# Performance work log

Measured on AMD Instinct MI355X. Metric: run time of the kernel, lower is better.

The kernel has to match this reference:

```python
import jax, jax.numpy as jnp
import numpy as np

N_NODES = 100000

def _gcn_norm(edge_index, num_nodes):
    # PyG GCNConv: add self-loops, symmetric normalization deg^-1/2 A_hat deg^-1/2
    loop = jnp.arange(num_nodes, dtype=edge_index.dtype)
    src = jnp.concatenate([edge_index[0], loop])  # [E+N]
    dst = jnp.concatenate([edge_index[1], loop])  # [E+N]
    deg = jax.ops.segment_sum(jnp.ones(dst.shape[0], jnp.float32), dst, num_segments=num_nodes)
    dis = jnp.where(deg > 0, jax.lax.rsqrt(deg), 0.0)
    norm = dis[src] * dis[dst]  # [E+N]
    return src, dst, norm

def _gcn_layer(x, W, b, src, dst, norm, num_nodes):
    xw = x @ W                                   # [N, H] dense GEMM first (out_dim <= in_dim)
    msg = xw[src] * norm[:, None]                # gather + scale per edge
    out = jax.ops.segment_sum(msg, dst, num_segments=num_nodes)  # scatter-add
    return out + b

def setup_inputs() -> dict:
    key = jax.random.key(0)
    ks = jax.random.split(key, 6)
    E = 1600000
    return {
        "x": jax.random.normal(ks[0], (N_NODES, 512), jnp.float32),
        "edge_index": jax.random.randint(ks[1], (2, E), 0, N_NODES, dtype=jnp.int64),
        "W1": jax.random.normal(ks[2], (512, 256), jnp.float32) * 0.04,
        "b1": jnp.zeros((256,), jnp.float32),
        "W2": jax.random.normal(ks[3], (256, 256), jnp.float32) * 0.06,
        "b2": jnp.zeros((256,), jnp.float32),
        "fc_w": jax.random.normal(ks[4], (256, 128), jnp.float32) * 0.06,
        "fc_b": jnp.zeros((128,), jnp.float32),
    }

def reference(x, edge_index, W1, b1, W2, b2, fc_w, fc_b):
    src, dst, norm = _gcn_norm(edge_index, N_NODES)
    h = jax.nn.relu(_gcn_layer(x, W1, b1, src, dst, norm, N_NODES))
    h = jax.nn.relu(_gcn_layer(h, W2, b2, src, dst, norm, N_NODES))
    return h @ fc_w + fc_b
```

## Files before the change

kernel.cpp:

```cpp
#include <hip/hip_runtime.h>


#define N_NODES 100000
constexpr int D_IN  = 512;
constexpr int D_H   = 256;
constexpr int D_OUT = 128;
constexpr int M_PAD = 100096;

typedef _Float16 f16x8 __attribute__((ext_vector_type(8)));
typedef _Float16 f16x4 __attribute__((ext_vector_type(4)));
typedef float f32x4 __attribute__((ext_vector_type(4)));

#define GLD16(SRC, DST) __builtin_amdgcn_global_load_lds(                      \
    (const __attribute__((address_space(1))) void*)(SRC),                      \
    (__attribute__((address_space(3))) void*)(DST), 16, 0, 0)

__global__ __launch_bounds__(256) void cvt_x_k(const float* __restrict__ x,
                                               _Float16* __restrict__ x16) {
  size_t i = ((size_t)blockIdx.x * 256 + threadIdx.x) * 8;
  const size_t valid = (size_t)N_NODES * D_IN;
  if (i < valid) {
    float4 a = *(const float4*)(x + i);
    float4 b = *(const float4*)(x + i + 4);
    f16x8 v;
    v[0] = (_Float16)a.x; v[1] = (_Float16)a.y;
    v[2] = (_Float16)a.z; v[3] = (_Float16)a.w;
    v[4] = (_Float16)b.x; v[5] = (_Float16)b.y;
    v[6] = (_Float16)b.z; v[7] = (_Float16)b.w;
    *(f16x8*)(x16 + i) = v;
  } else if (i < (size_t)M_PAD * D_IN) {
    *(f16x8*)(x16 + i) = (f16x8){0, 0, 0, 0, 0, 0, 0, 0};
  }
}

__global__ __launch_bounds__(256) void deg_count_k(const int* __restrict__ dst,
                                                   int* __restrict__ deg,
                                                   int* __restrict__ pe, int E) {
  int i = (blockIdx.x * 256 + threadIdx.x) * 4;
  if (i + 3 < E) {
    int4 d = *(const int4*)(dst + i);
    int4 p;
    p.x = atomicAdd(&deg[d.x], 1);
    p.y = atomicAdd(&deg[d.y], 1);
    p.z = atomicAdd(&deg[d.z], 1);
    p.w = atomicAdd(&deg[d.w], 1);
    *(int4*)(pe + i) = p;
  } else {
    for (int t = i; t < E; ++t) pe[t] = atomicAdd(&deg[dst[t]], 1);
  }
}

__global__ __launch_bounds__(256) void scan1_k(const int* __restrict__ deg,
                                               int* __restrict__ off,
                                               int* __restrict__ bsum,
                                               float* __restrict__ dis, int n) {
  __shared__ int ts[256];
  const int tid = threadIdx.x;
  const int base = blockIdx.x * 1024 + tid * 4;
  int v[4];
#pragma unroll
  for (int t = 0; t < 4; ++t) v[t] = (base + t < n) ? deg[base + t] : 0;
#pragma unroll
  for (int t = 0; t < 4; ++t)
    if (base + t < n) dis[base + t] = rsqrtf((float)v[t] + 1.0f);
  const int tot = v[0] + v[1] + v[2] + v[3];
  ts[tid] = tot;
  __syncthreads();
  for (int o = 1; o < 256; o <<= 1) {
    int t = (tid >= o) ? ts[tid - o] : 0;
    __syncthreads();
    ts[tid] += t;
    __syncthreads();
  }
  int run = ts[tid] - tot;
#pragma unroll
  for (int t = 0; t < 4; ++t) {
    if (base + t < n) off[base + t] = run;
    run += v[t];
  }
  if (tid == 255) bsum[blockIdx.x] = ts[255];
}

__global__ __launch_bounds__(128) void scan2_k(int* __restrict__ bsum, int nb) {
  __shared__ int ts[128];
  const int tid = threadIdx.x;
  const int v = (tid < nb) ? bsum[tid] : 0;
  ts[tid] = v;
  __syncthreads();
  for (int o = 1; o < 128; o <<= 1) {
    int t = (tid >= o) ? ts[tid - o] : 0;
    __syncthreads();
    ts[tid] += t;
    __syncthreads();
  }
  if (tid < nb) bsum[tid] = ts[tid] - v;
}

__global__ __launch_bounds__(256) void fill_k(const int* __restrict__ src,
                                              const int* __restrict__ dst,
                                              const int* __restrict__ pe,
                                              const int* __restrict__ off,
                                              const int* __restrict__ bsum,
                                              int* __restrict__ ssorted, int E) {
  int i = (blockIdx.x * 256 + threadIdx.x) * 4;
  if (i + 3 < E) {
    int4 s = *(const int4*)(src + i);
    int4 d = *(const int4*)(dst + i);
    int4 p = *(const int4*)(pe + i);
    ssorted[off[d.x] + bsum[d.x >> 10] + p.x] = s.x;
    ssorted[off[d.y] + bsum[d.y >> 10] + p.y] = s.y;
    ssorted[off[d.z] + bsum[d.z >> 10] + p.z] = s.z;
    ssorted[off[d.w] + bsum[d.w >> 10] + p.w] = s.w;
  } else {
    for (int t = i; t < E; ++t) {
      int d = dst[t];
      ssorted[off[d] + bsum[d >> 10] + pe[t]] = src[t];
    }
  }
}

__global__ __launch_bounds__(256) void wtrans_all_k(const float* __restrict__ W1,
                                                    const float* __restrict__ W2,
                                                    const float* __restrict__ FC,
                                                    _Float16* __restrict__ w1t,
                                                    _Float16* __restrict__ w2t,
                                                    _Float16* __restrict__ fct) {
  int i = blockIdx.x * 256 + threadIdx.x;
  if (i < 131072) {
    int k = i >> 8, n = i & 255;
    w1t[(size_t)n * 512 + k] = (_Float16)W1[i];
  } else if (i < 196608) {
    int j = i - 131072;
    int k = j >> 8, n = j & 255;
    w2t[(size_t)n * 256 + k] = (_Float16)W2[j];
  } else if (i < 229376) {
    int j = i - 196608;
    int k = j >> 7, n = j & 127;
    fct[(size_t)n * 256 + k] = (_Float16)FC[j];
  }
}

template<int BN, bool OUT_Y>
__global__ __launch_bounds__(512, 4) void gemm_glds_k(
    const _Float16* __restrict__ A16,
    const _Float16* __restrict__ Bt,
    const float* __restrict__ bias,
    const float* __restrict__ dis,
    float* __restrict__ C,
    _Float16* __restrict__ Y,
    int M, int K) {
  constexpr int BM = 128, BK = 32;
  constexpr int FN  = BN / 64;
  constexpr int NBI = BN / 128;
  constexpr int ASZ = BM * BK;
  constexpr int BSZ = BN * BK;
  constexpr int EPAD = 4;

  __shared__ __align__(16) _Float16 smem[2 * (ASZ + BSZ)];
  _Float16* As = smem;
  _Float16* Bs = smem + 2 * ASZ;
  float* epi = (float*)smem;

  const int tid  = threadIdx.x;
  const int w    = tid >> 6, lane = tid & 63;
  const int wm   = w >> 2, wn = w & 3;
  const int l15  = lane & 15, l16 = lane >> 4;
  const int row0 = blockIdx.y * BM;

  const int lr = lane >> 2, lg = lane & 3;
  const int arow  = w * 16 + lr;
  const int brow0 = w * (NBI * 16) + lr;
  const int brow1 = brow0 + 16;
  const _Float16* srcA  = A16 + (size_t)(row0 + arow) * K + ((lg ^ (arow & 3)) << 3);
  const _Float16* srcB0 = Bt + (size_t)brow0 * K + ((lg ^ (brow0 & 3)) << 3);
  const _Float16* srcB1 = Bt + (size_t)brow1 * K + ((lg ^ (brow1 & 3)) << 3);
  _Float16* dstA  = &As[(w * 16) * BK];
  _Float16* dstB0 = &Bs[(w * (NBI * 16)) * BK];
  _Float16* dstB1 = &Bs[(w * (NBI * 16) + 16) * BK];

  f32x4 acc[4][FN];
#pragma unroll
  for (int i = 0; i < 4; ++i)
#pragma unroll
    for (int j = 0; j < FN; ++j) acc[i][j] = (f32x4){0.f, 0.f, 0.f, 0.f};

  const int nsteps = K >> 5;

  auto stage = [&](int t) {
    const int kt = t << 5;
    const int pa = (t & 1) * ASZ, pb = (t & 1) * BSZ;
    GLD16(srcA + kt, dstA + pa);
    GLD16(srcB0 + kt, dstB0 + pb);
    if constexpr (NBI == 2) GLD16(srcB1 + kt, dstB1 + pb);
  };

  stage(0);
  __syncthreads();

  for (int t = 0; t < nsteps; ++t) {
    if (t + 1 < nsteps) stage(t + 1);
    const _Float16* as = As + (t & 1) * ASZ;
    const _Float16* bs = Bs + (t & 1) * BSZ;
    f16x8 a[4], b[FN];
#pragma unroll
    for (int i = 0; i < 4; ++i) {
      const int r = wm * 64 + i * 16 + l15;
      a[i] = *(const f16x8*)&as[r * BK + ((l16 ^ (r & 3)) << 3)];
    }
#pragma unroll
    for (int j = 0; j < FN; ++j) {
      const int n = wn * (FN * 16) + j * 16 + l15;
      b[j] = *(const f16x8*)&bs[n * BK + ((l16 ^ (n & 3)) << 3)];
    }
#pragma unroll
    for (int i = 0; i < 4; ++i)
#pragma unroll
      for (int j = 0; j < FN; ++j)
        acc[i][j] = __builtin_amdgcn_mfma_f32_16x16x32_f16(a[i], b[j], acc[i][j], 0, 0, 0);
    __syncthreads();
  }

  constexpr int ESTR = BN + EPAD;
  constexpr int CPT  = BN / 16;
#pragma unroll
  for (int c = 0; c < 4; ++c) {
    if (wm == (c >> 1)) {
      const int ib = (c & 1) * 2;
#pragma unroll
      for (int ii = 0; ii < 2; ++ii) {
        const int i = ib + ii;
#pragma unroll
        for (int j = 0; j < FN; ++j) {
          const int col = wn * (FN * 16) + j * 16 + l15;
#pragma unroll
          for (int r = 0; r < 4; ++r) {
            const int lrow = ii * 16 + l16 * 4 + r;
            epi[lrow * ESTR + col] = acc[i][j][r];
          }
        }
      }
    }
    __syncthreads();
    {
      const int lrow = tid >> 4;
      const int grow = row0 + c * 32 + lrow;
      const int colb = (tid & 15) * CPT;
      if (grow < M) {
        float v[CPT];
#pragma unroll
        for (int q = 0; q < CPT; q += 4)
          *(float4*)&v[q] = *(const float4*)&epi[lrow * ESTR + colb + q];
        if constexpr (OUT_Y) {
          const float dv = dis[grow];
          f16x8 o[CPT / 8];
#pragma unroll
          for (int q = 0; q < CPT; ++q) o[q >> 3][q & 7] = (_Float16)(v[q] * dv);
#pragma unroll
          for (int q = 0; q < CPT / 8; ++q)
            *(f16x8*)(Y + (size_t)grow * BN + colb + q * 8) = o[q];
        } else {
#pragma unroll
          for (int q = 0; q < CPT; ++q) v[q] += bias[colb + q];
#pragma unroll
          for (int q = 0; q < CPT; q += 4)
            *(float4*)(C + (size_t)grow * BN + colb + q) = *(const float4*)&v[q];
        }
      }
    }
    __syncthreads();
  }
}

__global__ __launch_bounds__(256) void gather_k(const _Float16* __restrict__ y,
                                                const int* __restrict__ ssorted,
                                                const int* __restrict__ off,
                                                const int* __restrict__ bsum,
                                                const float* __restrict__ dis,
                                                const float* __restrict__ bias,
                                                _Float16* __restrict__ h,
                                                int n, int E) {
  const int gid = blockIdx.x * 256 + threadIdx.x;
  const int v = gid >> 6, lane = gid & 63;
  if (v >= n) return;

  const float dv = dis[v];
  const int fo = lane * 4;

  f16x4 sv = *(const f16x4*)(y + (size_t)v * 256 + fo);
  float4 acc = make_float4((float)sv[0], (float)sv[1], (float)sv[2], (float)sv[3]);

  const int beg = off[v] + bsum[v >> 10];
  const int end = (v + 1 < n) ? (off[v + 1] + bsum[(v + 1) >> 10]) : E;
  const int ne = end - beg;

  for (int j0 = 0; j0 < ne; j0 += 64) {
    const int rem = ne - j0;
    const int cnt = rem < 64 ? rem : 64;
    int s_l = 0;
    if (lane < cnt) s_l = ssorted[beg + j0 + lane];

    int k = 0;
    for (; k + 8 <= cnt; k += 8) {
      f16x4 yv[8];
#pragma unroll
      for (int u = 0; u < 8; ++u) {
        const int s = __shfl(s_l, k + u);
        yv[u] = *(const f16x4*)(y + (size_t)s * 256 + fo);
      }
#pragma unroll
      for (int u = 0; u < 8; ++u) {
        acc.x += (float)yv[u][0];
        acc.y += (float)yv[u][1];
        acc.z += (float)yv[u][2];
        acc.w += (float)yv[u][3];
      }
    }
    for (; k < cnt; ++k) {
      const int s = __shfl(s_l, k);
      const f16x4 yv = *(const f16x4*)(y + (size_t)s * 256 + fo);
      acc.x += (float)yv[0];
      acc.y += (float)yv[1];
      acc.z += (float)yv[2];
      acc.w += (float)yv[3];
    }
  }

  const float4 b = *(const float4*)(bias + fo);
  f16x4 o;
  o[0] = (_Float16)fmaxf(fmaf(dv, acc.x, b.x), 0.f);
  o[1] = (_Float16)fmaxf(fmaf(dv, acc.y, b.y), 0.f);
  o[2] = (_Float16)fmaxf(fmaf(dv, acc.z, b.z), 0.f);
  o[3] = (_Float16)fmaxf(fmaf(dv, acc.w, b.w), 0.f);
  *(f16x4*)(h + (size_t)v * 256 + fo) = o;
}

extern "C" void kernel_launch(void* const* d_in, const int* in_sizes, int n_in,
                              void* d_out, int out_size, void* d_ws, size_t ws_size,
                              hipStream_t stream) {
  const float* x    = (const float*)d_in[0];
  const int*   ei   = (const int*)d_in[1];
  const float* W1   = (const float*)d_in[2];
  const float* b1   = (const float*)d_in[3];
  const float* W2   = (const float*)d_in[4];
  const float* b2   = (const float*)d_in[5];
  const float* fc_w = (const float*)d_in[6];
  const float* fc_b = (const float*)d_in[7];
  float* out = (float*)d_out;

  const int E = in_sizes[1] / 2;
  const int* src = ei;
  const int* dst = ei + E;
  const int N = N_NODES;

  char* p = (char*)d_ws;
  int*   deg     = (int*)p;            p += (size_t)N * 4;
  float* dis     = (float*)p;          p += (size_t)N * 4;
  int*   off     = (int*)p;            p += (size_t)(N + 1) * 4;
  int*   pe      = (int*)p;            p += (size_t)E * 4;
  int*   ssorted = (int*)p;            p += (size_t)E * 4;
  int*   bsum    = (int*)p;            p += 512;
  p = (char*)(((size_t)p + 255) & ~(size_t)255);
  _Float16* w1t = (_Float16*)p;        p += (size_t)D_H   * D_IN * 2;
  _Float16* w2t = (_Float16*)p;        p += (size_t)D_H   * D_H  * 2;
  _Float16* fct = (_Float16*)p;        p += (size_t)D_OUT * D_H  * 2;
  p = (char*)(((size_t)p + 255) & ~(size_t)255);
  _Float16* x16 = (_Float16*)p;        p += (size_t)M_PAD * D_IN * 2;
  _Float16* y16 = (_Float16*)p;        p += (size_t)M_PAD * D_H * 2;
  _Float16* h16 = (_Float16*)p;        p += (size_t)M_PAD * D_H * 2;

  cvt_x_k<<<(M_PAD * (D_IN / 8) + 255) / 256, 256, 0, stream>>>(x, x16);
  wtrans_all_k<<<896, 256, 0, stream>>>(W1, W2, fc_w, w1t, w2t, fct);

  const int NB1 = (N + 1023) / 1024;
  const int EB4 = ((E + 3) / 4 + 255) / 256;
  hipMemsetAsync(deg, 0, N * sizeof(int), stream);
  deg_count_k<<<EB4, 256, 0, stream>>>(dst, deg, pe, E);
  scan1_k<<<NB1, 256, 0, stream>>>(deg, off, bsum, dis, N);
  scan2_k<<<1, 128, 0, stream>>>(bsum, NB1);
  fill_k<<<EB4, 256, 0, stream>>>(src, dst, pe, off, bsum, ssorted, E);

  const int node_wave_blocks = (N * 64 + 255) / 256;
  const dim3 gg(1, M_PAD / 128);

  gemm_glds_k<256, true><<<gg, 512, 0, stream>>>(
      x16, w1t, nullptr, dis, nullptr, y16, N, D_IN);
  gather_k<<<node_wave_blocks, 256, 0, stream>>>(y16, ssorted, off, bsum, dis, b1, h16, N, E);

  gemm_glds_k<256, true><<<gg, 512, 0, stream>>>(
      h16, w2t, nullptr, dis, nullptr, y16, N, D_H);
  gather_k<<<node_wave_blocks, 256, 0, stream>>>(y16, ssorted, off, bsum, dis, b2, h16, N, E);

  gemm_glds_k<128, false><<<gg, 512, 0, stream>>>(
      h16, fct, fc_b, nullptr, out, nullptr, N, D_H);
}
```

Measured before the change: 505.4 us.

## Triple-buffer GEMM LDS staging with prefetch depth two and vmcnt waits

Switches the fp16 MFMA GEMM from double to triple-buffered LDS tiles and issues global->LDS loads two K-steps ahead. Explicit s_waitcnt vmcnt counts plus a single barrier per step replace the trailing __syncthreads, so load latency can overlap more compute. This raises LDS use by half, which may reduce occupancy under launch_bounds(512,4). The hand-written vmcnt values also rely on the exact number of outstanding loads.

```diff
diff --git a/kernel.cpp b/kernel.cpp
--- a/kernel.cpp
+++ b/kernel.cpp
@@ -156,9 +156,9 @@
   constexpr int BSZ = BN * BK;
   constexpr int EPAD = 4;
 
-  __shared__ __align__(16) _Float16 smem[2 * (ASZ + BSZ)];
+  __shared__ __align__(16) _Float16 smem[3 * (ASZ + BSZ)];
   _Float16* As = smem;
-  _Float16* Bs = smem + 2 * ASZ;
+  _Float16* Bs = smem + 3 * ASZ;
   float* epi = (float*)smem;
 
   const int tid  = threadIdx.x;
@@ -186,21 +186,33 @@
 
   const int nsteps = K >> 5;
 
-  auto stage = [&](int t) {
+  auto stage = [&](int t, int buf) {
     const int kt = t << 5;
-    const int pa = (t & 1) * ASZ, pb = (t & 1) * BSZ;
-    GLD16(srcA + kt, dstA + pa);
-    GLD16(srcB0 + kt, dstB0 + pb);
-    if constexpr (NBI == 2) GLD16(srcB1 + kt, dstB1 + pb);
+    GLD16(srcA + kt, dstA + buf * ASZ);
+    GLD16(srcB0 + kt, dstB0 + buf * BSZ);
+    if constexpr (NBI == 2) GLD16(srcB1 + kt, dstB1 + buf * BSZ);
   };
 
-  stage(0);
-  __syncthreads();
-
+  stage(0, 0);
+  if (nsteps > 1) stage(1, 1);
+
+  int rbuf = 0;
+  int wbuf = 2;
   for (int t = 0; t < nsteps; ++t) {
-    if (t + 1 < nsteps) stage(t + 1);
-    const _Float16* as = As + (t & 1) * ASZ;
-    const _Float16* bs = Bs + (t & 1) * BSZ;
+    if (t + 1 < nsteps) {
+      if constexpr (NBI == 2) asm volatile("s_waitcnt vmcnt(3)" ::: "memory");
+      else                    asm volatile("s_waitcnt vmcnt(2)" ::: "memory");
+    } else {
+      asm volatile("s_waitcnt vmcnt(0)" ::: "memory");
+    }
+    __builtin_amdgcn_sched_barrier(0);
+    __builtin_amdgcn_s_barrier();
+    __builtin_amdgcn_sched_barrier(0);
+
+    if (t + 2 < nsteps) stage(t + 2, wbuf);
+
+    const _Float16* as = As + rbuf * ASZ;
+    const _Float16* bs = Bs + rbuf * BSZ;
     f16x8 a[4], b[FN];
 #pragma unroll
     for (int i = 0; i < 4; ++i) {
@@ -217,8 +229,11 @@
 #pragma unroll
       for (int j = 0; j < FN; ++j)
         acc[i][j] = __builtin_amdgcn_mfma_f32_16x16x32_f16(a[i], b[j], acc[i][j], 0, 0, 0);
-    __syncthreads();
-  }
+
+    rbuf = (rbuf == 2) ? 0 : rbuf + 1;
+    wbuf = (wbuf == 2) ? 0 : wbuf + 1;
+  }
+  __syncthreads();
 
   constexpr int ESTR = BN + EPAD;
   constexpr int CPT  = BN / 16;
```

Result: no change. 500.7 us (-0.9%).
